# Kernel tuning notes

Hardware: AMD Instinct MI355X
Metric: run time of the kernel (lower is better)

Reference implementation:

```python
import jax, jax.numpy as jnp
import numpy as np
import math

N, H, D_MODEL = 2048, 16, 2048
D_K = D_MODEL // H
D_FF = 4 * D_MODEL
EPS = 1e-5


def _layernorm(x, alpha, beta):
    # torch: mean/var over dim=1 (=feature dim for 2D input), unbiased=False
    m = jnp.mean(x, axis=1, keepdims=True)
    v = jnp.var(x, axis=1, keepdims=True)
    return (x - m) / jnp.sqrt(v + EPS) * alpha + beta


def setup_inputs() -> dict:
    key = jax.random.key(0)
    ks = jax.random.split(key, 12)
    s = 0.02  # weight init scale
    return {
        "X": jax.random.normal(ks[0], (N, D_MODEL), jnp.float32),
        "Wq": jax.random.normal(ks[1], (H, D_MODEL, D_K), jnp.float32) * s,
        "bq": jax.random.normal(ks[2], (H, D_K), jnp.float32) * s,
        "Wk": jax.random.normal(ks[3], (H, D_MODEL, D_K), jnp.float32) * s,
        "bk": jax.random.normal(ks[4], (H, D_K), jnp.float32) * s,
        "Wv": jax.random.normal(ks[5], (H, D_MODEL, D_K), jnp.float32) * s,
        "bv": jax.random.normal(ks[6], (H, D_K), jnp.float32) * s,
        "alpha1": jnp.ones((N, D_MODEL), jnp.float32),
        "beta1": jnp.zeros((N, D_MODEL), jnp.float32),
        "W1": jax.random.normal(ks[7], (D_MODEL, D_FF), jnp.float32) * s,
        "b1": jax.random.normal(ks[8], (D_FF,), jnp.float32) * s,
        "W2": jax.random.normal(ks[9], (D_FF, D_MODEL), jnp.float32) * s,
        "b2": jax.random.normal(ks[10], (D_MODEL,), jnp.float32) * s,
        "alpha2": jnp.ones((N, D_MODEL), jnp.float32),
        "beta2": jnp.zeros((N, D_MODEL), jnp.float32),
    }


def reference(X, Wq, bq, Wk, bk, Wv, bv, alpha1, beta1, W1, b1, W2, b2, alpha2, beta2):
    # --- Multi-headed self-attention (h per-head linears fused as stacked weights) ---
    Q = jnp.einsum('nd,hdk->hnk', X, Wq) + bq[:, None, :]  # (H, N, D_K)
    K = jnp.einsum('nd,hdk->hnk', X, Wk) + bk[:, None, :]
    V = jnp.einsum('nd,hdk->hnk', X, Wv) + bv[:, None, :]
    scores = jnp.einsum('hnk,hmk->hnm', Q, K) / math.sqrt(D_K)  # (H, N, N)
    A = jax.nn.softmax(scores, axis=-1)  # softmax over keys (torch dim=1 of 2D)
    O = jnp.einsum('hnm,hmk->hnk', A, V)  # (H, N, D_K)
    attn = jnp.transpose(O, (1, 0, 2)).reshape(N, D_MODEL)  # concat heads on dim=1
    # --- Add & Norm 1 (dropout is identity at inference) ---
    h1 = _layernorm(X + attn, alpha1, beta1)
    # --- FFN ---
    ffn = jnp.maximum(h1 @ W1 + b1, 0.0) @ W2 + b2
    # --- Add & Norm 2 ---
    return _layernorm(h1 + ffn, alpha2, beta2)
```

## Files before the change

kernel.cpp:

```cpp
#include <hip/hip_runtime.h>
#include <hip/hip_bf16.h>

#define N_TOK 2048
#define DMODEL 2048
#define NH 16
#define DK 128
#define DFF 8192

typedef __attribute__((ext_vector_type(8))) short short8;
typedef __attribute__((ext_vector_type(4))) short s16x4;
typedef __attribute__((ext_vector_type(4))) float f32x4;

__device__ __forceinline__ short f2bf(float f) {
    unsigned int x = __builtin_bit_cast(unsigned int, f);
    unsigned int r = (x + 0x7fffu + ((x >> 16) & 1u)) >> 16;
    return (short)r;
}
__device__ __forceinline__ float bf2f(short s) {
    unsigned int u = ((unsigned int)(unsigned short)s) << 16;
    return __builtin_bit_cast(float, u);
}

__global__ __launch_bounds__(256) void cast_f32_bf16(const float* __restrict__ in,
                                                     short* __restrict__ out, int n8) {
    int i = blockIdx.x * 256 + threadIdx.x;
    if (i >= n8) return;
    const float4* p = (const float4*)in + (size_t)i * 2;
    float4 a = p[0], b = p[1];
    short8 o;
    o[0] = f2bf(a.x); o[1] = f2bf(a.y); o[2] = f2bf(a.z); o[3] = f2bf(a.w);
    o[4] = f2bf(b.x); o[5] = f2bf(b.y); o[6] = f2bf(b.z); o[7] = f2bf(b.w);
    *(short8*)(out + (size_t)i * 8) = o;
}

template <typename TIN>
__global__ __launch_bounds__(256) void transpose_cast(const TIN* __restrict__ in,
                                                      short* __restrict__ out,
                                                      int R, int C, long sIn, long sOut) {
    __shared__ float t[64][65];
    in  += (long)blockIdx.z * sIn;
    out += (long)blockIdx.z * sOut;
    const int tid = threadIdx.x;
    long r0 = (long)blockIdx.y * 64, c0 = (long)blockIdx.x * 64;
    if constexpr (sizeof(TIN) == 4) {
#pragma unroll
        for (int i = 0; i < 4; i++) {
            int r = (tid >> 4) + i * 16;
            int c = (tid & 15) * 4;
            float4 v = *(const float4*)((const float*)in + (r0 + r) * (long)C + c0 + c);
            t[r][c + 0] = v.x; t[r][c + 1] = v.y; t[r][c + 2] = v.z; t[r][c + 3] = v.w;
        }
    } else {
#pragma unroll
        for (int i = 0; i < 2; i++) {
            int r = (tid >> 3) + i * 32;
            int c = (tid & 7) * 8;
            short8 v = *(const short8*)((const short*)in + (r0 + r) * (long)C + c0 + c);
#pragma unroll
            for (int j = 0; j < 8; j++) t[r][c + j] = bf2f(v[j]);
        }
    }
    __syncthreads();
#pragma unroll
    for (int p = 0; p < 2; p++) {
        int c = (tid >> 3) + p * 32;
        int r8 = (tid & 7) * 8;
        short8 v;
#pragma unroll
        for (int j = 0; j < 8; j++) v[j] = f2bf(t[r8 + j][c]);
        *(short8*)(out + (c0 + c) * (long)R + r0 + r8) = v;
    }
}

__device__ __forceinline__ void gld_lds16(const void* g, void* l) {
    __builtin_amdgcn_global_load_lds(
        (const __attribute__((address_space(1))) void*)g,
        (__attribute__((address_space(3))) void*)l, 16, 0, 0);
}

#define VM8 asm volatile("s_waitcnt vmcnt(8)" ::: "memory")
#define VM0 asm volatile("s_waitcnt vmcnt(0)" ::: "memory")
#define VMNONE ((void)0)

#define PHASE(BUF, MH, NHI, RA, RBNH, STAGE_STMT, VMSTMT)                       \
  {                                                                             \
    if (RA) {                                                                   \
      _Pragma("unroll") for (int mp = 0; mp < 4; mp++)                          \
        _Pragma("unroll") for (int kk = 0; kk < 2; kk++) {                      \
          int rowA = wr * 128 + (MH) * 64 + mp * 16 + fr;                       \
          af[mp][kk] = *(const short8*)((const char*)lds + (BUF) * 65536 +      \
                         rowA * 128 + (((kk * 4 + fq) ^ (rowA & 7)) << 4));     \
        }                                                                       \
    }                                                                           \
    if ((RBNH) < 2) {                                                           \
      _Pragma("unroll") for (int np = 0; np < 2; np++)                          \
        _Pragma("unroll") for (int kk = 0; kk < 2; kk++) {                      \
          int rowB = wc * 64 + (RBNH) * 32 + np * 16 + fr;                      \
          bf[(RBNH) & 1][np][kk] =                                              \
              *(const short8*)((const char*)lds + (BUF) * 65536 + 32768 +       \
                  rowB * 128 + (((kk * 4 + fq) ^ (rowB & 7)) << 4));            \
        }                                                                       \
    }                                                                           \
    STAGE_STMT;                                                                 \
    __builtin_amdgcn_s_barrier();                                               \
    __builtin_amdgcn_s_setprio(1);                                              \
    _Pragma("unroll") for (int mp = 0; mp < 4; mp++)                            \
      _Pragma("unroll") for (int np = 0; np < 2; np++)                          \
        _Pragma("unroll") for (int kk = 0; kk < 2; kk++)                        \
          acc[(MH) * 4 + mp][(NHI) * 2 + np] =                                  \
              __builtin_amdgcn_mfma_f32_16x16x32_bf16(                          \
                  af[mp][kk], bf[NHI][np][kk], acc[(MH) * 4 + mp][(NHI) * 2 + np],\
                  0, 0, 0);                                                     \
    __builtin_amdgcn_s_setprio(0);                                              \
    VMSTMT;                                                                     \
    __builtin_amdgcn_s_barrier();                                               \
  }

template <int MODE>
__global__ __launch_bounds__(512, 2) void gemm256(const short* __restrict__ A,
                                                  const short* __restrict__ Bt,
                                                  void* __restrict__ Cv,
                                                  const float* __restrict__ b0,
                                                  const float* __restrict__ b1,
                                                  const float* __restrict__ b2,
                                                  int Ktot, int TM) {
    __shared__ short lds[65536];
    const int tid = threadIdx.x, lane = tid & 63, w = tid >> 6;
    const int T = gridDim.x, bid = blockIdx.x;
    const int vbid = (bid & 7) * (T >> 3) + (bid >> 3);
    const int mt = vbid % TM;
    const int rest = vbid / TM;
    int nt = rest, z = 0;
    if (MODE == 2) { nt = rest & 7; z = rest >> 3; }
    const long brow = (long)mt * 256, bcol = (long)nt * 256;
    const short* Ab = A + (MODE == 2 ? (long)z * 2048 : 0);
    const short* Bb = Bt + (MODE == 2 ? (long)z * 2048 : 0);

    auto stageA = [&](int kt, int buf, int mh) {
#pragma unroll
        for (int j = 0; j < 2; j++) {
            int row = mh * 64 + j * 128 + (tid >> 3);
            int g = (lane & 7) ^ (row & 7);
            gld_lds16((const char*)(Ab + (brow + row) * (long)Ktot + (long)kt * 64) + g * 16,
                      (char*)lds + buf * 65536 + mh * 8192 + j * 16384 + w * 1024 + lane * 16);
        }
    };
    auto stageB = [&](int kt, int buf, int nh) {
#pragma unroll
        for (int j = 0; j < 2; j++) {
            int s = 2 * j + (w >> 2);
            int rin = (w & 3) * 8 + (lane >> 3);
            int row = s * 64 + nh * 32 + rin;
            int g = (lane & 7) ^ (row & 7);
            gld_lds16((const char*)(Bb + (bcol + row) * (long)Ktot + (long)kt * 64) + g * 16,
                      (char*)lds + buf * 65536 + 32768 + j * 16384 + (w >> 2) * 8192 +
                          nh * 4096 + (w & 3) * 1024 + lane * 16);
        }
    };

    const int wr = w >> 2, wc = w & 3;
    const int fr = lane & 15, fq = lane >> 4;
    f32x4 acc[8][4] = {};
    short8 af[4][2], bf[2][2][2];

    stageA(0, 0, 0); stageB(0, 0, 0); stageB(0, 0, 1); stageA(0, 0, 1);
    stageA(1, 1, 0); stageB(1, 1, 0); stageB(1, 1, 1); stageA(1, 1, 1);
    VM8;
    __builtin_amdgcn_s_barrier();

    for (int i = 0; i < 15; i++) {
        const int kn = 2 * i + 2;
        PHASE(0, 0, 0, 1, 0, {}, VMNONE)
        PHASE(0, 0, 1, 0, 1, { stageA(kn, 0, 0); stageB(kn, 0, 0); }, VMNONE)
        PHASE(0, 1, 0, 1, 2, { stageB(kn, 0, 1); }, VMNONE)
        PHASE(0, 1, 1, 0, 2, { stageA(kn, 0, 1); }, VM8)
        PHASE(1, 0, 0, 1, 0, {}, VMNONE)
        PHASE(1, 0, 1, 0, 1, { stageA(kn + 1, 1, 0); stageB(kn + 1, 1, 0); }, VMNONE)
        PHASE(1, 1, 0, 1, 2, { stageB(kn + 1, 1, 1); }, VMNONE)
        PHASE(1, 1, 1, 0, 2, { stageA(kn + 1, 1, 1); }, VM8)
    }
    PHASE(0, 0, 0, 1, 0, {}, VMNONE)
    PHASE(0, 0, 1, 0, 1, {}, VMNONE)
    PHASE(0, 1, 0, 1, 2, {}, VMNONE)
    PHASE(0, 1, 1, 0, 2, {}, VM0)
    PHASE(1, 0, 0, 1, 0, {}, VMNONE)
    PHASE(1, 0, 1, 0, 1, {}, VMNONE)
    PHASE(1, 1, 0, 1, 2, {}, VMNONE)
    PHASE(1, 1, 1, 0, 2, {}, VMNONE)

    const long crow0 = brow + wr * 128, ccol0 = bcol + wc * 64;
#pragma unroll
    for (int n = 0; n < 4; n++) {
        const long col = ccol0 + (n >> 1) * 32 + (n & 1) * 16 + fr;
        float bval = 0.f;
        if (MODE == 0) {
            const float* bp = (col >> 11) == 0 ? b0 : (col >> 11) == 1 ? b1 : b2;
            bval = bp[col & 2047];
        } else if (MODE == 1) bval = b0[col];
#pragma unroll
        for (int m = 0; m < 8; m++) {
#pragma unroll
            for (int r = 0; r < 4; r++) {
                const long row = crow0 + (m >> 2) * 64 + (m & 3) * 16 + fq * 4 + r;
                float v = acc[m][n][r] + bval;
                if (MODE == 0) {
                    const long slab = col >> 7;
                    ((short*)Cv)[slab * (2048L * 128) + row * 128 + (col & 127)] = f2bf(v);
                } else if (MODE == 1) {
                    ((short*)Cv)[row * 8192 + col] = f2bf(fmaxf(v, 0.f));
                } else {
                    ((short*)Cv)[(long)z * (2048L * 2048) + row * 2048 + col] = f2bf(v);
                }
            }
        }
    }
}

__global__ __launch_bounds__(512, 2) void attn_flash(const short* __restrict__ Q,
                                                     const short* __restrict__ Kc,
                                                     const short* __restrict__ VT,
                                                     float* __restrict__ O) {
    __shared__ short lds[73728];
    const int tid = threadIdx.x, lane = tid & 63, w = tid >> 6;
    const int bid = blockIdx.x;
    const int vid = (bid & 7) * 32 + (bid >> 3);
    const int h = vid >> 4, qt = vid & 15;
    const int fr = lane & 15, fq = lane >> 4;
    const long qbase = (long)qt * 128 + w * 16;
    const short* Qh = Q  + (long)h * N_TOK * DK;
    const short* Kh = Kc + (long)h * N_TOK * DK;
    const short* Vh = VT + (long)h * DK * N_TOK;
    short* Pw = lds + 65536 + w * 1024;

    short8 qf[4];
#pragma unroll
    for (int c = 0; c < 4; c++)
        qf[c] = *(const short8*)(Qh + (qbase + fr) * DK + c * 32 + fq * 8);

    float mrow = -1e30f, lrow = 0.f;
    f32x4 oacc[8] = {};
    const float C1 = 0.08838834764831845f * 1.4426950408889634f;

    int wr_off[4], rd_off[2];
#pragma unroll
    for (int jc = 0; jc < 4; jc++)
        wr_off[jc] = (fr * 64 + jc * 16 + fq * 4) ^ ((fr & 7) << 3);
#pragma unroll
    for (int kc = 0; kc < 2; kc++)
        rd_off[kc] = (fr * 64 + kc * 32 + fq * 8) ^ ((fr & 7) << 3);
    int colKb[4], colVb[2];
#pragma unroll
    for (int c = 0; c < 4; c++) colKb[c] = (c * 64 + fq * 16) ^ ((fr & 7) << 4);
#pragma unroll
    for (int kc = 0; kc < 2; kc++) colVb[kc] = (kc * 64 + fq * 16) ^ ((fr & 7) << 4);

    auto stageK = [&](int kvt) {
        const int buf = kvt & 3;
        const char* Kg = (const char*)(Kh + (long)kvt * 64 * DK);
        char* Kd = (char*)lds + buf * 16384;
#pragma unroll
        for (int i = 0; i < 2; i++) {
            int a = (w * 2 + i) * 1024 + (lane << 4);
            int src = a ^ (((a >> 8) & 7) << 4);
            gld_lds16(Kg + src, Kd + (w * 2 + i) * 1024);
        }
    };
    auto stageV = [&](int kvt) {
        const int buf = kvt & 3;
        char* Vd = (char*)lds + 65536 + buf * 16384;
#pragma unroll
        for (int i = 0; i < 2; i++) {
            int a = (w * 2 + i) * 1024 + (lane << 4);
            int row = a >> 7;
            int inner = (a & 127) ^ ((row & 7) << 4);
            const char* src = (const char*)Vh + ((long)row * N_TOK + (long)kvt * 64) * 2 + inner;
            gld_lds16(src, Vd + (w * 2 + i) * 1024);
        }
    };

    const int NT = N_TOK / 64;
    stageK(0); stageV(0); stageK(1); stageV(1); stageK(2); stageV(2); stageK(3);
    asm volatile("s_waitcnt vmcnt(12)" ::: "memory");
    __builtin_amdgcn_s_barrier();
    __builtin_amdgcn_sched_barrier(0);

    for (int t = 0; t < NT; t++) {
        const char* Kcb = (const char*)lds + (t & 3) * 16384;
        f32x4 s[4] = {};
#pragma unroll
        for (int jc = 0; jc < 4; jc++) {
            const char* rb = Kcb + (jc * 16 + fr) * 256;
#pragma unroll
            for (int c = 0; c < 4; c++) {
                short8 kf = *(const short8*)(rb + colKb[c]);
                s[jc] = __builtin_amdgcn_mfma_f32_16x16x32_bf16(kf, qf[c], s[jc], 0, 0, 0);
            }
        }

        float tm = -1e30f;
#pragma unroll
        for (int jc = 0; jc < 4; jc++)
#pragma unroll
            for (int r = 0; r < 4; r++) tm = fmaxf(tm, s[jc][r]);
        tm = fmaxf(tm, __shfl_xor(tm, 16));
        tm = fmaxf(tm, __shfl_xor(tm, 32));
        float nm = fmaxf(mrow, tm);
        float resc = exp2f(C1 * (mrow - nm));
        mrow = nm;
        float sum = 0.f;
#pragma unroll
        for (int jc = 0; jc < 4; jc++)
#pragma unroll
            for (int r = 0; r < 4; r++) {
                float p = exp2f(C1 * (s[jc][r] - nm));
                s[jc][r] = p;
                sum += p;
            }
        sum += __shfl_xor(sum, 16);
        sum += __shfl_xor(sum, 32);
        lrow = lrow * resc + sum;
#pragma unroll
        for (int f = 0; f < 8; f++)
#pragma unroll
            for (int r = 0; r < 4; r++) oacc[f][r] *= resc;

#pragma unroll
        for (int jc = 0; jc < 4; jc++) {
            s16x4 pk;
            pk[0] = f2bf(s[jc][0]); pk[1] = f2bf(s[jc][1]);
            pk[2] = f2bf(s[jc][2]); pk[3] = f2bf(s[jc][3]);
            *(s16x4*)(Pw + wr_off[jc]) = pk;
        }
        short8 pa[2];
#pragma unroll
        for (int kc = 0; kc < 2; kc++)
            pa[kc] = *(const short8*)(Pw + rd_off[kc]);

        if (t < NT - 4) asm volatile("s_waitcnt vmcnt(8)" ::: "memory");
        else            asm volatile("s_waitcnt vmcnt(0)" ::: "memory");
        __builtin_amdgcn_sched_barrier(0);
        __builtin_amdgcn_s_barrier();
        __builtin_amdgcn_sched_barrier(0);

        const char* Vcb = (const char*)lds + 65536 + (t & 3) * 16384;
#pragma unroll
        for (int f = 0; f < 8; f++) {
            const char* rb = Vcb + (f * 16 + fr) * 128;
#pragma unroll
            for (int kc = 0; kc < 2; kc++) {
                short8 vf = *(const short8*)(rb + colVb[kc]);
                oacc[f] = __builtin_amdgcn_mfma_f32_16x16x32_bf16(vf, pa[kc], oacc[f], 0, 0, 0);
            }
        }

        if (t + 4 < NT) stageK(t + 4);
        if (t + 3 < NT) stageV(t + 3);
    }

    const float inv = 1.f / lrow;
    const long row = qbase + fr;
#pragma unroll
    for (int f = 0; f < 8; f++) {
        float4 o;
        o.x = oacc[f][0] * inv; o.y = oacc[f][1] * inv;
        o.z = oacc[f][2] * inv; o.w = oacc[f][3] * inv;
        *(float4*)(O + row * (long)DMODEL + h * DK + f * 16 + fq * 4) = o;
    }
}

template <bool WBF>
__global__ __launch_bounds__(256) void add_ln(const float* __restrict__ A,
                                              const float* __restrict__ B,
                                              const float* __restrict__ alpha,
                                              const float* __restrict__ beta,
                                              float* __restrict__ out,
                                              short* __restrict__ outbf) {
    const int row = blockIdx.x, t = threadIdx.x;
    const long base = (long)row * DMODEL;
    float4 va[2], vb[2];
    float s = 0.f, q = 0.f;
#pragma unroll
    for (int i = 0; i < 2; i++) {
        long off = base + (long)(t + i * 256) * 4;
        va[i] = *(const float4*)(A + off);
        vb[i] = *(const float4*)(B + off);
        float x0 = va[i].x + vb[i].x, x1 = va[i].y + vb[i].y;
        float x2 = va[i].z + vb[i].z, x3 = va[i].w + vb[i].w;
        s += x0 + x1 + x2 + x3;
        q += x0 * x0 + x1 * x1 + x2 * x2 + x3 * x3;
    }
#pragma unroll
    for (int o = 1; o < 64; o <<= 1) { s += __shfl_xor(s, o); q += __shfl_xor(q, o); }
    __shared__ float red[8];
    if ((t & 63) == 0) { red[t >> 6] = s; red[4 + (t >> 6)] = q; }
    __syncthreads();
    s = red[0] + red[1] + red[2] + red[3];
    q = red[4] + red[5] + red[6] + red[7];
    const float mean = s * (1.f / DMODEL);
    const float var = q * (1.f / DMODEL) - mean * mean;
    const float rstd = rsqrtf(var + 1e-5f);
#pragma unroll
    for (int i = 0; i < 2; i++) {
        long off = base + (long)(t + i * 256) * 4;
        float4 al = *(const float4*)(alpha + off);
        float4 be = *(const float4*)(beta + off);
        float x[4] = { va[i].x + vb[i].x, va[i].y + vb[i].y, va[i].z + vb[i].z, va[i].w + vb[i].w };
        float a[4] = { al.x, al.y, al.z, al.w };
        float b[4] = { be.x, be.y, be.z, be.w };
#pragma unroll
        for (int j = 0; j < 4; j++) {
            float o2 = (x[j] - mean) * rstd * a[j] + b[j];
            out[off + j] = o2;
            if (WBF) outbf[off + j] = f2bf(o2);
        }
    }
}

__global__ __launch_bounds__(256) void add_ln2_red(const float* __restrict__ H1,
                                                   const short* __restrict__ F4,
                                                   const float* __restrict__ b2,
                                                   const float* __restrict__ alpha,
                                                   const float* __restrict__ beta,
                                                   float* __restrict__ out) {
    const int row = blockIdx.x, t = threadIdx.x;
    const long base = (long)row * DMODEL;
    const long SL = (long)N_TOK * DMODEL;
    float x[8];
    float s = 0.f, q = 0.f;
#pragma unroll
    for (int i = 0; i < 2; i++) {
        long off = base + (long)(t + i * 256) * 4;
        int col = (t + i * 256) * 4;
        float4 a  = *(const float4*)(H1 + off);
        s16x4 f0 = *(const s16x4*)(F4 + off);
        s16x4 f1 = *(const s16x4*)(F4 + off + SL);
        s16x4 f2 = *(const s16x4*)(F4 + off + 2 * SL);
        s16x4 f3 = *(const s16x4*)(F4 + off + 3 * SL);
        float4 bb = *(const float4*)(b2 + col);
        float xa[4] = { a.x + bb.x, a.y + bb.y, a.z + bb.z, a.w + bb.w };
#pragma unroll
        for (int j = 0; j < 4; j++) {
            float v = xa[j] + bf2f(f0[j]) + bf2f(f1[j]) + bf2f(f2[j]) + bf2f(f3[j]);
            x[i * 4 + j] = v;
            s += v; q += v * v;
        }
    }
#pragma unroll
    for (int o = 1; o < 64; o <<= 1) { s += __shfl_xor(s, o); q += __shfl_xor(q, o); }
    __shared__ float red[8];
    if ((t & 63) == 0) { red[t >> 6] = s; red[4 + (t >> 6)] = q; }
    __syncthreads();
    s = red[0] + red[1] + red[2] + red[3];
    q = red[4] + red[5] + red[6] + red[7];
    const float mean = s * (1.f / DMODEL);
    const float var = q * (1.f / DMODEL) - mean * mean;
    const float rstd = rsqrtf(var + 1e-5f);
#pragma unroll
    for (int i = 0; i < 2; i++) {
        long off = base + (long)(t + i * 256) * 4;
        float4 al = *(const float4*)(alpha + off);
        float4 be = *(const float4*)(beta + off);
        float a[4] = { al.x, al.y, al.z, al.w };
        float b[4] = { be.x, be.y, be.z, be.w };
#pragma unroll
        for (int j = 0; j < 4; j++)
            out[off + j] = (x[i * 4 + j] - mean) * rstd * a[j] + b[j];
    }
}

extern "C" void kernel_launch(void* const* d_in, const int* in_sizes, int n_in,
                              void* d_out, int out_size, void* d_ws, size_t ws_size,
                              hipStream_t stream) {
    const float* X      = (const float*)d_in[0];
    const float* Wq     = (const float*)d_in[1];
    const float* bq     = (const float*)d_in[2];
    const float* Wk     = (const float*)d_in[3];
    const float* bk     = (const float*)d_in[4];
    const float* Wv     = (const float*)d_in[5];
    const float* bv     = (const float*)d_in[6];
    const float* alpha1 = (const float*)d_in[7];
    const float* beta1  = (const float*)d_in[8];
    const float* W1     = (const float*)d_in[9];
    const float* b1     = (const float*)d_in[10];
    const float* W2     = (const float*)d_in[11];
    const float* b2     = (const float*)d_in[12];
    const float* alpha2 = (const float*)d_in[13];
    const float* beta2  = (const float*)d_in[14];
    float* out = (float*)d_out;

    char* ws = (char*)d_ws;
    size_t off = 0;
    auto alloc = [&](size_t bytes) -> void* {
        void* p = ws + off;
        off += (bytes + 255) & ~(size_t)255;
        return p;
    };
    short* XBF   = (short*)alloc(2048UL * 2048 * 2);
    short* WQKVT = (short*)alloc(48UL * 128 * 2048 * 2);
    short* W1T   = (short*)alloc(8192UL * 2048 * 2);
    short* W2T   = (short*)alloc(2048UL * 8192 * 2);
    short* QKV   = (short*)alloc(48UL * 2048 * 128 * 2);
    short* VT    = (short*)alloc(16UL * 128 * 2048 * 2);
    float* ATTN  = (float*)alloc(2048UL * 2048 * 4);
    float* H1    = (float*)alloc(2048UL * 2048 * 4);
    short* H1BF  = (short*)alloc(2048UL * 2048 * 2);
    short* G     = (short*)alloc(2048UL * 8192 * 2);
    short* F4 = XBF;

    cast_f32_bf16<<<2048, 256, 0, stream>>>(X, XBF, 2048 * 2048 / 8);
    transpose_cast<float><<<dim3(2, 32, 16), 256, 0, stream>>>(Wq, WQKVT,                    2048, 128, 2048L * 128, 128L * 2048);
    transpose_cast<float><<<dim3(2, 32, 16), 256, 0, stream>>>(Wk, WQKVT + 16L * 128 * 2048, 2048, 128, 2048L * 128, 128L * 2048);
    transpose_cast<float><<<dim3(2, 32, 16), 256, 0, stream>>>(Wv, WQKVT + 32L * 128 * 2048, 2048, 128, 2048L * 128, 128L * 2048);
    transpose_cast<float><<<dim3(128, 32, 1), 256, 0, stream>>>(W1, W1T, 2048, 8192, 0, 0);
    transpose_cast<float><<<dim3(32, 128, 1), 256, 0, stream>>>(W2, W2T, 8192, 2048, 0, 0);

    gemm256<0><<<192, 512, 0, stream>>>(XBF, WQKVT, QKV, bq, bk, bv, 2048, 8);

    transpose_cast<__hip_bfloat16><<<dim3(2, 32, 16), 256, 0, stream>>>(
        (const __hip_bfloat16*)(QKV + 32L * 2048 * 128), VT, 2048, 128, 2048L * 128, 128L * 2048);

    attn_flash<<<256, 512, 0, stream>>>(QKV, QKV + 16L * 2048 * 128, VT, ATTN);

    add_ln<true><<<2048, 256, 0, stream>>>(X, ATTN, alpha1, beta1, H1, H1BF);

    gemm256<1><<<256, 512, 0, stream>>>(H1BF, W1T, G, b1, nullptr, nullptr, 2048, 8);
    gemm256<2><<<256, 512, 0, stream>>>(G, W2T, F4, nullptr, nullptr, nullptr, 8192, 8);

    add_ln2_red<<<2048, 256, 0, stream>>>(H1, F4, b2, alpha2, beta2, out);
}
```

Measured before the change: 368.2 us.

## Replace pipelined 256x256 GEMM with simple single-buffered 256x128 GEMM kernel

Swaps the double-buffered, phase-interleaved 256x256 GEMM (512 threads, 128KB LDS) for a simpler 256x128 tile kernel with 256 threads, a K-step of 32, a single LDS buffer and a sync before and after each step. Grid sizes double for all three GEMM launches. This raises block count and occupancy and cuts LDS use, but it drops the overlap between global loads and MFMA compute and adds more barriers per K element. MODE 2 split-K indexing is adapted to 16 column tiles.

Measured after the change: 402.6 us. 1.09x slower.

```diff
diff --git a/kernel.cpp b/kernel.cpp
--- a/kernel.cpp
+++ b/kernel.cpp
@@ -78,120 +78,76 @@
         (__attribute__((address_space(3))) void*)l, 16, 0, 0);
 }
 
-#define VM8 asm volatile("s_waitcnt vmcnt(8)" ::: "memory")
-#define VM0 asm volatile("s_waitcnt vmcnt(0)" ::: "memory")
-#define VMNONE ((void)0)
-
-#define PHASE(BUF, MH, NHI, RA, RBNH, STAGE_STMT, VMSTMT)                       \
-  {                                                                             \
-    if (RA) {                                                                   \
-      _Pragma("unroll") for (int mp = 0; mp < 4; mp++)                          \
-        _Pragma("unroll") for (int kk = 0; kk < 2; kk++) {                      \
-          int rowA = wr * 128 + (MH) * 64 + mp * 16 + fr;                       \
-          af[mp][kk] = *(const short8*)((const char*)lds + (BUF) * 65536 +      \
-                         rowA * 128 + (((kk * 4 + fq) ^ (rowA & 7)) << 4));     \
-        }                                                                       \
-    }                                                                           \
-    if ((RBNH) < 2) {                                                           \
-      _Pragma("unroll") for (int np = 0; np < 2; np++)                          \
-        _Pragma("unroll") for (int kk = 0; kk < 2; kk++) {                      \
-          int rowB = wc * 64 + (RBNH) * 32 + np * 16 + fr;                      \
-          bf[(RBNH) & 1][np][kk] =                                              \
-              *(const short8*)((const char*)lds + (BUF) * 65536 + 32768 +       \
-                  rowB * 128 + (((kk * 4 + fq) ^ (rowB & 7)) << 4));            \
-        }                                                                       \
-    }                                                                           \
-    STAGE_STMT;                                                                 \
-    __builtin_amdgcn_s_barrier();                                               \
-    __builtin_amdgcn_s_setprio(1);                                              \
-    _Pragma("unroll") for (int mp = 0; mp < 4; mp++)                            \
-      _Pragma("unroll") for (int np = 0; np < 2; np++)                          \
-        _Pragma("unroll") for (int kk = 0; kk < 2; kk++)                        \
-          acc[(MH) * 4 + mp][(NHI) * 2 + np] =                                  \
-              __builtin_amdgcn_mfma_f32_16x16x32_bf16(                          \
-                  af[mp][kk], bf[NHI][np][kk], acc[(MH) * 4 + mp][(NHI) * 2 + np],\
-                  0, 0, 0);                                                     \
-    __builtin_amdgcn_s_setprio(0);                                              \
-    VMSTMT;                                                                     \
-    __builtin_amdgcn_s_barrier();                                               \
-  }
-
 template <int MODE>
-__global__ __launch_bounds__(512, 2) void gemm256(const short* __restrict__ A,
+__global__ __launch_bounds__(256, 2) void gemm_cr(const short* __restrict__ A,
                                                   const short* __restrict__ Bt,
                                                   void* __restrict__ Cv,
                                                   const float* __restrict__ b0,
                                                   const float* __restrict__ b1,
                                                   const float* __restrict__ b2,
                                                   int Ktot, int TM) {
-    __shared__ short lds[65536];
+    __shared__ short lds[12288];
     const int tid = threadIdx.x, lane = tid & 63, w = tid >> 6;
     const int T = gridDim.x, bid = blockIdx.x;
     const int vbid = (bid & 7) * (T >> 3) + (bid >> 3);
     const int mt = vbid % TM;
     const int rest = vbid / TM;
     int nt = rest, z = 0;
-    if (MODE == 2) { nt = rest & 7; z = rest >> 3; }
-    const long brow = (long)mt * 256, bcol = (long)nt * 256;
+    if (MODE == 2) { nt = rest & 15; z = rest >> 4; }
+    const long brow = (long)mt * 256, bcol = (long)nt * 128;
     const short* Ab = A + (MODE == 2 ? (long)z * 2048 : 0);
     const short* Bb = Bt + (MODE == 2 ? (long)z * 2048 : 0);
 
-    auto stageA = [&](int kt, int buf, int mh) {
-#pragma unroll
-        for (int j = 0; j < 2; j++) {
-            int row = mh * 64 + j * 128 + (tid >> 3);
-            int g = (lane & 7) ^ (row & 7);
-            gld_lds16((const char*)(Ab + (brow + row) * (long)Ktot + (long)kt * 64) + g * 16,
-                      (char*)lds + buf * 65536 + mh * 8192 + j * 16384 + w * 1024 + lane * 16);
+    auto stage = [&](int kt) {
+        const long k0 = (long)kt * 32;
+#pragma unroll
+        for (int i = 0; i < 4; i++) {
+            int a = i * 4096 + tid * 16;
+            int row = a >> 6;
+            int colb = (a & 63) ^ (((row >> 1) & 3) << 4);
+            gld_lds16((const char*)(Ab + (brow + row) * (long)Ktot + k0) + colb,
+                      (char*)lds + a);
+        }
+#pragma unroll
+        for (int i = 0; i < 2; i++) {
+            int a = i * 4096 + tid * 16;
+            int row = a >> 6;
+            int colb = (a & 63) ^ (((row >> 1) & 3) << 4);
+            gld_lds16((const char*)(Bb + (bcol + row) * (long)Ktot + k0) + colb,
+                      (char*)lds + 16384 + a);
         }
     };
-    auto stageB = [&](int kt, int buf, int nh) {
-#pragma unroll
-        for (int j = 0; j < 2; j++) {
-            int s = 2 * j + (w >> 2);
-            int rin = (w & 3) * 8 + (lane >> 3);
-            int row = s * 64 + nh * 32 + rin;
-            int g = (lane & 7) ^ (row & 7);
-            gld_lds16((const char*)(Bb + (bcol + row) * (long)Ktot + (long)kt * 64) + g * 16,
-                      (char*)lds + buf * 65536 + 32768 + j * 16384 + (w >> 2) * 8192 +
-                          nh * 4096 + (w & 3) * 1024 + lane * 16);
-        }
-    };
-
-    const int wr = w >> 2, wc = w & 3;
+
+    const int wr = w >> 1, wc = w & 1;
     const int fr = lane & 15, fq = lane >> 4;
+    const int fcol = (fq * 16) ^ (((fr >> 1) & 3) << 4);
     f32x4 acc[8][4] = {};
-    short8 af[4][2], bf[2][2][2];
-
-    stageA(0, 0, 0); stageB(0, 0, 0); stageB(0, 0, 1); stageA(0, 0, 1);
-    stageA(1, 1, 0); stageB(1, 1, 0); stageB(1, 1, 1); stageA(1, 1, 1);
-    VM8;
-    __builtin_amdgcn_s_barrier();
-
-    for (int i = 0; i < 15; i++) {
-        const int kn = 2 * i + 2;
-        PHASE(0, 0, 0, 1, 0, {}, VMNONE)
-        PHASE(0, 0, 1, 0, 1, { stageA(kn, 0, 0); stageB(kn, 0, 0); }, VMNONE)
-        PHASE(0, 1, 0, 1, 2, { stageB(kn, 0, 1); }, VMNONE)
-        PHASE(0, 1, 1, 0, 2, { stageA(kn, 0, 1); }, VM8)
-        PHASE(1, 0, 0, 1, 0, {}, VMNONE)
-        PHASE(1, 0, 1, 0, 1, { stageA(kn + 1, 1, 0); stageB(kn + 1, 1, 0); }, VMNONE)
-        PHASE(1, 1, 0, 1, 2, { stageB(kn + 1, 1, 1); }, VMNONE)
-        PHASE(1, 1, 1, 0, 2, { stageA(kn + 1, 1, 1); }, VM8)
-    }
-    PHASE(0, 0, 0, 1, 0, {}, VMNONE)
-    PHASE(0, 0, 1, 0, 1, {}, VMNONE)
-    PHASE(0, 1, 0, 1, 2, {}, VMNONE)
-    PHASE(0, 1, 1, 0, 2, {}, VM0)
-    PHASE(1, 0, 0, 1, 0, {}, VMNONE)
-    PHASE(1, 0, 1, 0, 1, {}, VMNONE)
-    PHASE(1, 1, 0, 1, 2, {}, VMNONE)
-    PHASE(1, 1, 1, 0, 2, {}, VMNONE)
+
+    const int NT = 2048 / 32;
+    for (int t = 0; t < NT; t++) {
+        stage(t);
+        __syncthreads();
+        short8 af[8], bf[4];
+#pragma unroll
+        for (int m = 0; m < 8; m++)
+            af[m] = *(const short8*)((const char*)lds + (wr * 128 + m * 16 + fr) * 64 + fcol);
+#pragma unroll
+        for (int n = 0; n < 4; n++)
+            bf[n] = *(const short8*)((const char*)lds + 16384 + (wc * 64 + n * 16 + fr) * 64 + fcol);
+        __builtin_amdgcn_s_setprio(1);
+#pragma unroll
+        for (int m = 0; m < 8; m++)
+#pragma unroll
+            for (int n = 0; n < 4; n++)
+                acc[m][n] = __builtin_amdgcn_mfma_f32_16x16x32_bf16(af[m], bf[n], acc[m][n], 0, 0, 0);
+        __builtin_amdgcn_s_setprio(0);
+        __syncthreads();
+    }
 
     const long crow0 = brow + wr * 128, ccol0 = bcol + wc * 64;
 #pragma unroll
     for (int n = 0; n < 4; n++) {
-        const long col = ccol0 + (n >> 1) * 32 + (n & 1) * 16 + fr;
+        const long col = ccol0 + n * 16 + fr;
         float bval = 0.f;
         if (MODE == 0) {
             const float* bp = (col >> 11) == 0 ? b0 : (col >> 11) == 1 ? b1 : b2;
@@ -201,7 +157,7 @@
         for (int m = 0; m < 8; m++) {
 #pragma unroll
             for (int r = 0; r < 4; r++) {
-                const long row = crow0 + (m >> 2) * 64 + (m & 3) * 16 + fq * 4 + r;
+                const long row = crow0 + m * 16 + fq * 4 + r;
                 float v = acc[m][n][r] + bval;
                 if (MODE == 0) {
                     const long slab = col >> 7;
@@ -514,7 +470,7 @@
     transpose_cast<float><<<dim3(128, 32, 1), 256, 0, stream>>>(W1, W1T, 2048, 8192, 0, 0);
     transpose_cast<float><<<dim3(32, 128, 1), 256, 0, stream>>>(W2, W2T, 8192, 2048, 0, 0);
 
-    gemm256<0><<<192, 512, 0, stream>>>(XBF, WQKVT, QKV, bq, bk, bv, 2048, 8);
+    gemm_cr<0><<<384, 256, 0, stream>>>(XBF, WQKVT, QKV, bq, bk, bv, 2048, 8);
 
     transpose_cast<__hip_bfloat16><<<dim3(2, 32, 16), 256, 0, stream>>>(
         (const __hip_bfloat16*)(QKV + 32L * 2048 * 128), VT, 2048, 128, 2048L * 128, 128L * 2048);
@@ -523,8 +479,8 @@
 
     add_ln<true><<<2048, 256, 0, stream>>>(X, ATTN, alpha1, beta1, H1, H1BF);
 
-    gemm256<1><<<256, 512, 0, stream>>>(H1BF, W1T, G, b1, nullptr, nullptr, 2048, 8);
-    gemm256<2><<<256, 512, 0, stream>>>(G, W2T, F4, nullptr, nullptr, nullptr, 8192, 8);
+    gemm_cr<1><<<512, 256, 0, stream>>>(H1BF, W1T, G, b1, nullptr, nullptr, 2048, 8);
+    gemm_cr<2><<<512, 256, 0, stream>>>(G, W2T, F4, nullptr, nullptr, nullptr, 8192, 8);
 
     add_ln2_red<<<2048, 256, 0, stream>>>(H1, F4, b2, alpha2, beta2, out);
 }
```
